# Optimization experiments

Hardware: AMD Instinct MI355X
Metric: run time of the kernel (lower is better)

Reference implementation:

```python
import jax, jax.numpy as jnp
import numpy as np

EPS = 1e-8  # matches torch F.cosine_similarity eps


def setup_inputs() -> dict:
    key = jax.random.key(0)
    k1, = jax.random.split(key, 1)
    N, U, D = 512, 32, 512
    embeddings = jax.random.normal(k1, (N, U, D), dtype=jnp.float32)
    w = jnp.asarray(10.0, dtype=jnp.float32)  # init_w
    b = jnp.asarray(-5.0, dtype=jnp.float32)  # init_b
    return {"embeddings": embeddings, "w": w, "b": b}


def reference(embeddings, w, b):
    N, U, D = embeddings.shape
    # centroids per speaker (mean over utterances; module includes current utt)
    centroids = embeddings.mean(axis=1)  # (N, D)
    # cosine similarity via normalize + matmul
    e = embeddings.reshape(N * U, D)
    e_n = e / jnp.maximum(jnp.linalg.norm(e, axis=-1, keepdims=True), EPS)
    c_n = centroids / jnp.maximum(
        jnp.linalg.norm(centroids, axis=-1, keepdims=True), EPS)
    sim = (e_n @ c_n.T).reshape(N, U, N)  # (N, U, N)
    sim = w * sim + b
    logp = jax.nn.log_softmax(sim, axis=-1)  # (N, U, N)
    # pick logp[j, k, j] for every j, k
    diag = jnp.take_along_axis(
        logp, jnp.arange(N)[:, None, None], axis=2)[..., 0]  # (N, U)
    return -diag.mean()
```

## Files before the change

kernel.cpp:

```cpp
#include <hip/hip_runtime.h>
#include <math.h>

#define N_SPK 512
#define N_UTT 32
#define DIM   512
#define EPSN  1e-8f

typedef __attribute__((ext_vector_type(8))) short  short8;
typedef __attribute__((ext_vector_type(4))) float  f32x4;

__device__ inline unsigned short f2bf(float x) {
  unsigned int u = __builtin_bit_cast(unsigned int, x);
  unsigned int r = (u + 0x7fffu + ((u >> 16) & 1u)) >> 16;
  return (unsigned short)r;
}

#define CNK_ELEMS (N_SPK * DIM)

__global__ __launch_bounds__(256) void centroid_kernel(
    const float* __restrict__ emb, unsigned short* __restrict__ cnk) {
  int j = blockIdx.x, t = threadIdx.x;
  int c4 = t & 127, half = t >> 7;
  const float4* base = (const float4*)(emb + (size_t)j * N_UTT * DIM);
  float4 s = {0.f, 0.f, 0.f, 0.f};
#pragma unroll
  for (int u = 0; u < 16; ++u) {
    float4 v = base[(half + 2 * u) * 128 + c4];
    s.x += v.x; s.y += v.y; s.z += v.z; s.w += v.w;
  }
  __shared__ float4 comb[128];
  if (half) comb[c4] = s;
  __syncthreads();
  float4 m = {0.f, 0.f, 0.f, 0.f};
  float ss = 0.f;
  if (!half) {
    float4 o = comb[c4];
    m.x = (s.x + o.x) * (1.f / N_UTT);
    m.y = (s.y + o.y) * (1.f / N_UTT);
    m.z = (s.z + o.z) * (1.f / N_UTT);
    m.w = (s.w + o.w) * (1.f / N_UTT);
    ss = m.x * m.x + m.y * m.y + m.z * m.z + m.w * m.w;
  }
#pragma unroll
  for (int off = 32; off > 0; off >>= 1) ss += __shfl_xor(ss, off, 64);
  __shared__ float red[4];
  if ((t & 63) == 0) red[t >> 6] = ss;
  __syncthreads();
  float total = red[0] + red[1] + red[2] + red[3];
  float inv = 1.f / fmaxf(sqrtf(total), EPSN);
  if (!half) {
    int d0 = c4 * 4;
    int kc = d0 >> 5;
    unsigned short* p = cnk + ((size_t)kc * N_SPK + j) * 32 + (d0 & 31);
    p[0] = f2bf(m.x * inv); p[1] = f2bf(m.y * inv);
    p[2] = f2bf(m.z * inv); p[3] = f2bf(m.w * inv);
  }
}

__global__ __launch_bounds__(512, 4) void ge2e_kernel(
    const float* __restrict__ emb, const unsigned short* __restrict__ cnk,
    const float* __restrict__ wp, const float* __restrict__ bp,
    float* __restrict__ partials) {
  __shared__ __align__(16) unsigned short E[N_UTT * DIM];
  __shared__ float red[8][N_UTT][2];
  __shared__ float dred[8];

  int j = blockIdx.x;
  int t = threadIdx.x;
  int lane = t & 63, wid = t >> 6;
  int n15 = lane & 15, quad = lane >> 4;

#pragma unroll
  for (int r8 = 0; r8 < 4; ++r8) {
    int r = wid * 4 + r8;
    const float* rp = emb + ((size_t)j * N_UTT + r) * DIM + lane * 8;
    float4 v0 = *(const float4*)rp;
    float4 v1 = *(const float4*)(rp + 4);
    float ss = v0.x * v0.x + v0.y * v0.y + v0.z * v0.z + v0.w * v0.w +
               v1.x * v1.x + v1.y * v1.y + v1.z * v1.z + v1.w * v1.w;
#pragma unroll
    for (int off = 32; off > 0; off >>= 1) ss += __shfl_xor(ss, off, 64);
    float inv = 1.f / fmaxf(sqrtf(ss), EPSN);
    short8 pk;
    pk[0] = (short)f2bf(v0.x * inv); pk[1] = (short)f2bf(v0.y * inv);
    pk[2] = (short)f2bf(v0.z * inv); pk[3] = (short)f2bf(v0.w * inv);
    pk[4] = (short)f2bf(v1.x * inv); pk[5] = (short)f2bf(v1.y * inv);
    pk[6] = (short)f2bf(v1.z * inv); pk[7] = (short)f2bf(v1.w * inv);
    int sw = lane ^ (r & 7);
    *(short8*)&E[r * DIM + sw * 8] = pk;
  }
  __syncthreads();

  f32x4 acc[2][4];
#pragma unroll
  for (int mt = 0; mt < 2; ++mt)
#pragma unroll
    for (int nt = 0; nt < 4; ++nt) acc[mt][nt] = (f32x4){0.f, 0.f, 0.f, 0.f};

  for (int ks = 0; ks < 16; ++ks) {
    short8 b[4];
#pragma unroll
    for (int nt = 0; nt < 4; ++nt) {
      int c = wid * 64 + nt * 16 + n15;
      b[nt] = *(const short8*)(cnk + ((size_t)ks * N_SPK + c) * 32 + quad * 8);
    }
    short8 a[2];
#pragma unroll
    for (int mt = 0; mt < 2; ++mt) {
      int r = mt * 16 + n15;
      int sw = (ks * 4 + quad) ^ (r & 7);
      a[mt] = *(const short8*)&E[r * DIM + sw * 8];
    }
#pragma unroll
    for (int mt = 0; mt < 2; ++mt)
#pragma unroll
      for (int nt = 0; nt < 4; ++nt)
        acc[mt][nt] = __builtin_amdgcn_mfma_f32_16x16x32_bf16(
            a[mt], b[nt], acc[mt][nt], 0, 0, 0);
  }

  float w = *wp, bb = *bp;
  float dsum = 0.f;
#pragma unroll
  for (int mt = 0; mt < 2; ++mt)
#pragma unroll
    for (int nt = 0; nt < 4; ++nt) {
      int c = wid * 64 + nt * 16 + n15;
      bool isdiag = (c == j);
#pragma unroll
      for (int rg = 0; rg < 4; ++rg) {
        float v = fmaf(w, acc[mt][nt][rg], bb);
        acc[mt][nt][rg] = v;
        if (isdiag) dsum += v;
      }
    }

#pragma unroll
  for (int mt = 0; mt < 2; ++mt)
#pragma unroll
    for (int rg = 0; rg < 4; ++rg) {
      float m = -INFINITY;
#pragma unroll
      for (int nt = 0; nt < 4; ++nt) m = fmaxf(m, acc[mt][nt][rg]);
#pragma unroll
      for (int off = 1; off < 16; off <<= 1) m = fmaxf(m, __shfl_xor(m, off, 64));
      float s = 0.f;
#pragma unroll
      for (int nt = 0; nt < 4; ++nt) s += __expf(acc[mt][nt][rg] - m);
#pragma unroll
      for (int off = 1; off < 16; off <<= 1) s += __shfl_xor(s, off, 64);
      if (n15 == 0) {
        int r = mt * 16 + quad * 4 + rg;
        red[wid][r][0] = m;
        red[wid][r][1] = s;
      }
    }
#pragma unroll
  for (int off = 32; off > 0; off >>= 1) dsum += __shfl_xor(dsum, off, 64);
  if (lane == 0) dred[wid] = dsum;
  __syncthreads();

  if (t < 32) {
    float M = -INFINITY;
#pragma unroll
    for (int ww = 0; ww < 8; ++ww) M = fmaxf(M, red[ww][t][0]);
    float S = 0.f;
#pragma unroll
    for (int ww = 0; ww < 8; ++ww) S += red[ww][t][1] * __expf(red[ww][t][0] - M);
    float lse = M + __logf(S);
#pragma unroll
    for (int off = 16; off > 0; off >>= 1) lse += __shfl_xor(lse, off, 64);
    if (t == 0) {
      float d = dred[0] + dred[1] + dred[2] + dred[3] +
                dred[4] + dred[5] + dred[6] + dred[7];
      partials[j] = lse - d;
    }
  }
}

__global__ __launch_bounds__(512) void finalize_kernel(
    const float* __restrict__ partials, float* __restrict__ out) {
  int t = threadIdx.x;
  float v = partials[t];
#pragma unroll
  for (int off = 32; off > 0; off >>= 1) v += __shfl_xor(v, off, 64);
  __shared__ float r[8];
  if ((t & 63) == 0) r[t >> 6] = v;
  __syncthreads();
  if (t == 0) {
    float s = r[0] + r[1] + r[2] + r[3] + r[4] + r[5] + r[6] + r[7];
    out[0] = s * (1.f / (N_SPK * N_UTT));
  }
}

extern "C" void kernel_launch(void* const* d_in, const int* in_sizes, int n_in,
                              void* d_out, int out_size, void* d_ws, size_t ws_size,
                              hipStream_t stream) {
  const float* emb = (const float*)d_in[0];
  const float* wp  = (const float*)d_in[1];
  const float* bp  = (const float*)d_in[2];
  float* out = (float*)d_out;
  unsigned short* cnk = (unsigned short*)d_ws;
  float* partials = (float*)((char*)d_ws + (size_t)CNK_ELEMS * 2);

  centroid_kernel<<<N_SPK, 256, 0, stream>>>(emb, cnk);
  ge2e_kernel<<<N_SPK, 512, 0, stream>>>(emb, cnk, wp, bp, partials);
  finalize_kernel<<<1, 512, 0, stream>>>(partials, out);
}
```

Baseline: 97.33 us.

## Double ge2e block threads and fold finalize into last-block atomic reduction

The main kernel now runs 1024 threads (16 waves) per speaker block, so each wave handles 32 centroid columns and 2 normalization rows instead of 64 and 4. The separate finalize launch is removed: every block atomically increments a counter, which the centroid kernel resets, and the last block to arrive sums the partials and writes the output. This is meant to raise parallelism per block and save one kernel launch. In exchange it adds atomic and fence overhead, and the 1024-thread launch bound with 8 blocks requested may limit registers per thread.

```diff
diff --git a/kernel.cpp b/kernel.cpp
--- a/kernel.cpp
+++ b/kernel.cpp
@@ -18,8 +18,10 @@
 #define CNK_ELEMS (N_SPK * DIM)
 
 __global__ __launch_bounds__(256) void centroid_kernel(
-    const float* __restrict__ emb, unsigned short* __restrict__ cnk) {
+    const float* __restrict__ emb, unsigned short* __restrict__ cnk,
+    unsigned int* __restrict__ counter) {
   int j = blockIdx.x, t = threadIdx.x;
+  if (j == 0 && t == 0) *counter = 0;
   int c4 = t & 127, half = t >> 7;
   const float4* base = (const float4*)(emb + (size_t)j * N_UTT * DIM);
   float4 s = {0.f, 0.f, 0.f, 0.f};
@@ -57,13 +59,16 @@
   }
 }
 
-__global__ __launch_bounds__(512, 4) void ge2e_kernel(
+__global__ __launch_bounds__(1024, 8) void ge2e_kernel(
     const float* __restrict__ emb, const unsigned short* __restrict__ cnk,
     const float* __restrict__ wp, const float* __restrict__ bp,
-    float* __restrict__ partials) {
+    float* __restrict__ partials, unsigned int* __restrict__ counter,
+    float* __restrict__ out) {
   __shared__ __align__(16) unsigned short E[N_UTT * DIM];
-  __shared__ float red[8][N_UTT][2];
-  __shared__ float dred[8];
+  __shared__ float red[16][N_UTT][2];
+  __shared__ float dred[16];
+  __shared__ float nred[16];
+  __shared__ int amLast;
 
   int j = blockIdx.x;
   int t = threadIdx.x;
@@ -71,8 +76,8 @@
   int n15 = lane & 15, quad = lane >> 4;
 
 #pragma unroll
-  for (int r8 = 0; r8 < 4; ++r8) {
-    int r = wid * 4 + r8;
+  for (int r8 = 0; r8 < 2; ++r8) {
+    int r = wid * 2 + r8;
     const float* rp = emb + ((size_t)j * N_UTT + r) * DIM + lane * 8;
     float4 v0 = *(const float4*)rp;
     float4 v1 = *(const float4*)(rp + 4);
@@ -91,17 +96,18 @@
   }
   __syncthreads();
 
-  f32x4 acc[2][4];
+  f32x4 acc[2][2];
 #pragma unroll
   for (int mt = 0; mt < 2; ++mt)
 #pragma unroll
-    for (int nt = 0; nt < 4; ++nt) acc[mt][nt] = (f32x4){0.f, 0.f, 0.f, 0.f};
-
+    for (int nt = 0; nt < 2; ++nt) acc[mt][nt] = (f32x4){0.f, 0.f, 0.f, 0.f};
+
+#pragma unroll 4
   for (int ks = 0; ks < 16; ++ks) {
-    short8 b[4];
-#pragma unroll
-    for (int nt = 0; nt < 4; ++nt) {
-      int c = wid * 64 + nt * 16 + n15;
+    short8 b[2];
+#pragma unroll
+    for (int nt = 0; nt < 2; ++nt) {
+      int c = wid * 32 + nt * 16 + n15;
       b[nt] = *(const short8*)(cnk + ((size_t)ks * N_SPK + c) * 32 + quad * 8);
     }
     short8 a[2];
@@ -114,7 +120,7 @@
 #pragma unroll
     for (int mt = 0; mt < 2; ++mt)
 #pragma unroll
-      for (int nt = 0; nt < 4; ++nt)
+      for (int nt = 0; nt < 2; ++nt)
         acc[mt][nt] = __builtin_amdgcn_mfma_f32_16x16x32_bf16(
             a[mt], b[nt], acc[mt][nt], 0, 0, 0);
   }
@@ -124,8 +130,8 @@
 #pragma unroll
   for (int mt = 0; mt < 2; ++mt)
 #pragma unroll
-    for (int nt = 0; nt < 4; ++nt) {
-      int c = wid * 64 + nt * 16 + n15;
+    for (int nt = 0; nt < 2; ++nt) {
+      int c = wid * 32 + nt * 16 + n15;
       bool isdiag = (c == j);
 #pragma unroll
       for (int rg = 0; rg < 4; ++rg) {
@@ -141,12 +147,12 @@
     for (int rg = 0; rg < 4; ++rg) {
       float m = -INFINITY;
 #pragma unroll
-      for (int nt = 0; nt < 4; ++nt) m = fmaxf(m, acc[mt][nt][rg]);
+      for (int nt = 0; nt < 2; ++nt) m = fmaxf(m, acc[mt][nt][rg]);
 #pragma unroll
       for (int off = 1; off < 16; off <<= 1) m = fmaxf(m, __shfl_xor(m, off, 64));
       float s = 0.f;
 #pragma unroll
-      for (int nt = 0; nt < 4; ++nt) s += __expf(acc[mt][nt][rg] - m);
+      for (int nt = 0; nt < 2; ++nt) s += __expf(acc[mt][nt][rg] - m);
 #pragma unroll
       for (int off = 1; off < 16; off <<= 1) s += __shfl_xor(s, off, 64);
       if (n15 == 0) {
@@ -163,33 +169,41 @@
   if (t < 32) {
     float M = -INFINITY;
 #pragma unroll
-    for (int ww = 0; ww < 8; ++ww) M = fmaxf(M, red[ww][t][0]);
+    for (int ww = 0; ww < 16; ++ww) M = fmaxf(M, red[ww][t][0]);
     float S = 0.f;
 #pragma unroll
-    for (int ww = 0; ww < 8; ++ww) S += red[ww][t][1] * __expf(red[ww][t][0] - M);
+    for (int ww = 0; ww < 16; ++ww)
+      S += red[ww][t][1] * __expf(red[ww][t][0] - M);
     float lse = M + __logf(S);
 #pragma unroll
     for (int off = 16; off > 0; off >>= 1) lse += __shfl_xor(lse, off, 64);
     if (t == 0) {
-      float d = dred[0] + dred[1] + dred[2] + dred[3] +
-                dred[4] + dred[5] + dred[6] + dred[7];
+      float d = 0.f;
+#pragma unroll
+      for (int ww = 0; ww < 16; ++ww) d += dred[ww];
       partials[j] = lse - d;
     }
   }
-}
-
-__global__ __launch_bounds__(512) void finalize_kernel(
-    const float* __restrict__ partials, float* __restrict__ out) {
-  int t = threadIdx.x;
-  float v = partials[t];
-#pragma unroll
-  for (int off = 32; off > 0; off >>= 1) v += __shfl_xor(v, off, 64);
-  __shared__ float r[8];
-  if ((t & 63) == 0) r[t >> 6] = v;
-  __syncthreads();
+
   if (t == 0) {
-    float s = r[0] + r[1] + r[2] + r[3] + r[4] + r[5] + r[6] + r[7];
-    out[0] = s * (1.f / (N_SPK * N_UTT));
+    __threadfence();
+    unsigned int old = atomicAdd(counter, 1u);
+    amLast = (old == (unsigned int)(gridDim.x - 1));
+  }
+  __syncthreads();
+  if (amLast) {
+    __threadfence();
+    float v = (t < N_SPK) ? partials[t] : 0.f;
+#pragma unroll
+    for (int off = 32; off > 0; off >>= 1) v += __shfl_xor(v, off, 64);
+    if (lane == 0) nred[wid] = v;
+    __syncthreads();
+    if (t == 0) {
+      float s = 0.f;
+#pragma unroll
+      for (int ww = 0; ww < 16; ++ww) s += nred[ww];
+      out[0] = s * (1.f / (N_SPK * N_UTT));
+    }
   }
 }
 
@@ -202,8 +216,10 @@
   float* out = (float*)d_out;
   unsigned short* cnk = (unsigned short*)d_ws;
   float* partials = (float*)((char*)d_ws + (size_t)CNK_ELEMS * 2);
-
-  centroid_kernel<<<N_SPK, 256, 0, stream>>>(emb, cnk);
-  ge2e_kernel<<<N_SPK, 512, 0, stream>>>(emb, cnk, wp, bp, partials);
-  finalize_kernel<<<1, 512, 0, stream>>>(partials, out);
-}
+  unsigned int* counter =
+      (unsigned int*)((char*)d_ws + (size_t)CNK_ELEMS * 2 + N_SPK * 4);
+
+  centroid_kernel<<<N_SPK, 256, 0, stream>>>(emb, cnk, counter);
+  ge2e_kernel<<<N_SPK, 1024, 0, stream>>>(emb, cnk, wp, bp, partials, counter,
+                                          out);
+}
```

Result: slower. 108.0 us (+10.9%).

## Fold normalization into prep kernel, stage bf16 embeddings, fuse finalize via atomic counter

Applied to the files above, without the earlier changes.

A single prep kernel now computes each speaker's centroid and also writes the row-normalized bf16 embeddings (already swizzled) to a workspace buffer. The ge2e kernel then only copies those bf16 rows into LDS instead of reading fp32 and normalizing. The separate finalize launch is replaced by a last-block-done pattern using an atomic counter. This reads the fp32 embeddings once instead of twice and removes one kernel launch, but adds a 16 MB bf16 write and read-back plus threadfence/atomic overhead.

```diff
diff --git a/kernel.cpp b/kernel.cpp
--- a/kernel.cpp
+++ b/kernel.cpp
@@ -15,60 +15,21 @@
   return (unsigned short)r;
 }
 
-#define CNK_ELEMS (N_SPK * DIM)
-
-__global__ __launch_bounds__(256) void centroid_kernel(
-    const float* __restrict__ emb, unsigned short* __restrict__ cnk) {
+#define CNK_BYTES ((size_t)N_SPK * DIM * 2)
+#define EG_BYTES  ((size_t)N_SPK * N_UTT * DIM * 2)
+
+__global__ __launch_bounds__(512) void prep_kernel(
+    const float* __restrict__ emb, unsigned short* __restrict__ cnk,
+    unsigned short* __restrict__ Eg, unsigned int* __restrict__ counter) {
+  __shared__ float colsum[8][DIM];
+  __shared__ float nred[8];
   int j = blockIdx.x, t = threadIdx.x;
-  int c4 = t & 127, half = t >> 7;
-  const float4* base = (const float4*)(emb + (size_t)j * N_UTT * DIM);
-  float4 s = {0.f, 0.f, 0.f, 0.f};
-#pragma unroll
-  for (int u = 0; u < 16; ++u) {
-    float4 v = base[(half + 2 * u) * 128 + c4];
-    s.x += v.x; s.y += v.y; s.z += v.z; s.w += v.w;
-  }
-  __shared__ float4 comb[128];
-  if (half) comb[c4] = s;
-  __syncthreads();
-  float4 m = {0.f, 0.f, 0.f, 0.f};
-  float ss = 0.f;
-  if (!half) {
-    float4 o = comb[c4];
-    m.x = (s.x + o.x) * (1.f / N_UTT);
-    m.y = (s.y + o.y) * (1.f / N_UTT);
-    m.z = (s.z + o.z) * (1.f / N_UTT);
-    m.w = (s.w + o.w) * (1.f / N_UTT);
-    ss = m.x * m.x + m.y * m.y + m.z * m.z + m.w * m.w;
-  }
-#pragma unroll
-  for (int off = 32; off > 0; off >>= 1) ss += __shfl_xor(ss, off, 64);
-  __shared__ float red[4];
-  if ((t & 63) == 0) red[t >> 6] = ss;
-  __syncthreads();
-  float total = red[0] + red[1] + red[2] + red[3];
-  float inv = 1.f / fmaxf(sqrtf(total), EPSN);
-  if (!half) {
-    int d0 = c4 * 4;
-    int kc = d0 >> 5;
-    unsigned short* p = cnk + ((size_t)kc * N_SPK + j) * 32 + (d0 & 31);
-    p[0] = f2bf(m.x * inv); p[1] = f2bf(m.y * inv);
-    p[2] = f2bf(m.z * inv); p[3] = f2bf(m.w * inv);
-  }
-}
-
-__global__ __launch_bounds__(512, 4) void ge2e_kernel(
-    const float* __restrict__ emb, const unsigned short* __restrict__ cnk,
-    const float* __restrict__ wp, const float* __restrict__ bp,
-    float* __restrict__ partials) {
-  __shared__ __align__(16) unsigned short E[N_UTT * DIM];
-  __shared__ float red[8][N_UTT][2];
-  __shared__ float dred[8];
-
-  int j = blockIdx.x;
-  int t = threadIdx.x;
   int lane = t & 63, wid = t >> 6;
-  int n15 = lane & 15, quad = lane >> 4;
+  if (j == 0 && t == 0) *counter = 0;
+
+  float cs[8];
+#pragma unroll
+  for (int i = 0; i < 8; ++i) cs[i] = 0.f;
 
 #pragma unroll
   for (int r8 = 0; r8 < 4; ++r8) {
@@ -76,6 +37,8 @@
     const float* rp = emb + ((size_t)j * N_UTT + r) * DIM + lane * 8;
     float4 v0 = *(const float4*)rp;
     float4 v1 = *(const float4*)(rp + 4);
+    cs[0] += v0.x; cs[1] += v0.y; cs[2] += v0.z; cs[3] += v0.w;
+    cs[4] += v1.x; cs[5] += v1.y; cs[6] += v1.z; cs[7] += v1.w;
     float ss = v0.x * v0.x + v0.y * v0.y + v0.z * v0.z + v0.w * v0.w +
                v1.x * v1.x + v1.y * v1.y + v1.z * v1.z + v1.w * v1.w;
 #pragma unroll
@@ -87,8 +50,48 @@
     pk[4] = (short)f2bf(v1.x * inv); pk[5] = (short)f2bf(v1.y * inv);
     pk[6] = (short)f2bf(v1.z * inv); pk[7] = (short)f2bf(v1.w * inv);
     int sw = lane ^ (r & 7);
-    *(short8*)&E[r * DIM + sw * 8] = pk;
-  }
+    *(short8*)&Eg[((size_t)j * N_UTT + r) * DIM + sw * 8] = pk;
+  }
+  *(float4*)&colsum[wid][lane * 8] = (float4){cs[0], cs[1], cs[2], cs[3]};
+  *(float4*)&colsum[wid][lane * 8 + 4] = (float4){cs[4], cs[5], cs[6], cs[7]};
+  __syncthreads();
+
+  float c = 0.f;
+#pragma unroll
+  for (int ww = 0; ww < 8; ++ww) c += colsum[ww][t];
+  c *= (1.f / N_UTT);
+  float ss = c * c;
+#pragma unroll
+  for (int off = 32; off > 0; off >>= 1) ss += __shfl_xor(ss, off, 64);
+  if (lane == 0) nred[wid] = ss;
+  __syncthreads();
+  float total = nred[0] + nred[1] + nred[2] + nred[3] +
+                nred[4] + nred[5] + nred[6] + nred[7];
+  float cinv = 1.f / fmaxf(sqrtf(total), EPSN);
+  cnk[((size_t)(t >> 5) * N_SPK + j) * 32 + (t & 31)] = f2bf(c * cinv);
+}
+
+__global__ __launch_bounds__(512, 4) void ge2e_kernel(
+    const unsigned short* __restrict__ Eg,
+    const unsigned short* __restrict__ cnk,
+    const float* __restrict__ wp, const float* __restrict__ bp,
+    float* __restrict__ partials, unsigned int* __restrict__ counter,
+    float* __restrict__ out) {
+  __shared__ __align__(16) unsigned short E[N_UTT * DIM];
+  __shared__ float red[8][N_UTT][2];
+  __shared__ float dred[8];
+  __shared__ float nred[8];
+  __shared__ int amLast;
+
+  int j = blockIdx.x;
+  int t = threadIdx.x;
+  int lane = t & 63, wid = t >> 6;
+  int n15 = lane & 15, quad = lane >> 4;
+
+  const int4* src = (const int4*)(Eg + (size_t)j * N_UTT * DIM);
+  int4* dst = (int4*)E;
+#pragma unroll
+  for (int i = 0; i < 4; ++i) dst[i * 512 + t] = src[i * 512 + t];
   __syncthreads();
 
   f32x4 acc[2][4];
@@ -176,20 +179,25 @@
       partials[j] = lse - d;
     }
   }
-}
-
-__global__ __launch_bounds__(512) void finalize_kernel(
-    const float* __restrict__ partials, float* __restrict__ out) {
-  int t = threadIdx.x;
-  float v = partials[t];
-#pragma unroll
-  for (int off = 32; off > 0; off >>= 1) v += __shfl_xor(v, off, 64);
-  __shared__ float r[8];
-  if ((t & 63) == 0) r[t >> 6] = v;
-  __syncthreads();
+
   if (t == 0) {
-    float s = r[0] + r[1] + r[2] + r[3] + r[4] + r[5] + r[6] + r[7];
-    out[0] = s * (1.f / (N_SPK * N_UTT));
+    __threadfence();
+    unsigned int old = atomicAdd(counter, 1u);
+    amLast = (old == (unsigned int)(gridDim.x - 1));
+  }
+  __syncthreads();
+  if (amLast) {
+    __threadfence();
+    float v = partials[t];
+#pragma unroll
+    for (int off = 32; off > 0; off >>= 1) v += __shfl_xor(v, off, 64);
+    if (lane == 0) nred[wid] = v;
+    __syncthreads();
+    if (t == 0) {
+      float s = nred[0] + nred[1] + nred[2] + nred[3] +
+                nred[4] + nred[5] + nred[6] + nred[7];
+      out[0] = s * (1.f / (N_SPK * N_UTT));
+    }
   }
 }
 
@@ -201,9 +209,12 @@
   const float* bp  = (const float*)d_in[2];
   float* out = (float*)d_out;
   unsigned short* cnk = (unsigned short*)d_ws;
-  float* partials = (float*)((char*)d_ws + (size_t)CNK_ELEMS * 2);
-
-  centroid_kernel<<<N_SPK, 256, 0, stream>>>(emb, cnk);
-  ge2e_kernel<<<N_SPK, 512, 0, stream>>>(emb, cnk, wp, bp, partials);
-  finalize_kernel<<<1, 512, 0, stream>>>(partials, out);
-}
+  unsigned short* Eg  = (unsigned short*)((char*)d_ws + CNK_BYTES);
+  float* partials = (float*)((char*)d_ws + CNK_BYTES + EG_BYTES);
+  unsigned int* counter =
+      (unsigned int*)((char*)d_ws + CNK_BYTES + EG_BYTES + N_SPK * 4);
+
+  prep_kernel<<<N_SPK, 512, 0, stream>>>(emb, cnk, Eg, counter);
+  ge2e_kernel<<<N_SPK, 512, 0, stream>>>(Eg, cnk, wp, bp, partials, counter,
+                                         out);
+}
```

Result: slower. 112.0 us (+15.0%).

## Split similarity kernel across column halves and widen centroid blocks

Applied to the files above, without the earlier changes.

The main kernel now launches two blocks per speaker, each covering half of the centroid columns. Each block writes per-row partial max and sum-exp pairs, and the finalize kernel merges them into the log-sum-exp. The centroid kernel uses 1024 threads with an 8-way row split to spread its loads across more threads. The aim is more blocks to occupy the GPU, at the cost of reloading and normalizing each speaker's embeddings twice and a heavier finalize step.

```diff
diff --git a/kernel.cpp b/kernel.cpp
--- a/kernel.cpp
+++ b/kernel.cpp
@@ -15,42 +15,44 @@
   return (unsigned short)r;
 }
 
-#define CNK_ELEMS (N_SPK * DIM)
-
-__global__ __launch_bounds__(256) void centroid_kernel(
-    const float* __restrict__ emb, unsigned short* __restrict__ cnk) {
+#define CNK_BYTES ((size_t)N_SPK * DIM * 2)
+#define MS_BYTES  ((size_t)1024 * N_UTT * 2 * 4)
+
+__global__ void centroid_kernel(const float* __restrict__ emb,
+                                unsigned short* __restrict__ cnk) {
+  __shared__ float4 colsum[8][128];
+  __shared__ float nred[2];
   int j = blockIdx.x, t = threadIdx.x;
-  int c4 = t & 127, half = t >> 7;
+  int c4 = t & 127, rg = t >> 7;
   const float4* base = (const float4*)(emb + (size_t)j * N_UTT * DIM);
   float4 s = {0.f, 0.f, 0.f, 0.f};
 #pragma unroll
-  for (int u = 0; u < 16; ++u) {
-    float4 v = base[(half + 2 * u) * 128 + c4];
+  for (int u = 0; u < 4; ++u) {
+    float4 v = base[(rg + 8 * u) * 128 + c4];
     s.x += v.x; s.y += v.y; s.z += v.z; s.w += v.w;
   }
-  __shared__ float4 comb[128];
-  if (half) comb[c4] = s;
-  __syncthreads();
-  float4 m = {0.f, 0.f, 0.f, 0.f};
-  float ss = 0.f;
-  if (!half) {
-    float4 o = comb[c4];
-    m.x = (s.x + o.x) * (1.f / N_UTT);
-    m.y = (s.y + o.y) * (1.f / N_UTT);
-    m.z = (s.z + o.z) * (1.f / N_UTT);
-    m.w = (s.w + o.w) * (1.f / N_UTT);
-    ss = m.x * m.x + m.y * m.y + m.z * m.z + m.w * m.w;
-  }
-#pragma unroll
-  for (int off = 32; off > 0; off >>= 1) ss += __shfl_xor(ss, off, 64);
-  __shared__ float red[4];
-  if ((t & 63) == 0) red[t >> 6] = ss;
-  __syncthreads();
-  float total = red[0] + red[1] + red[2] + red[3];
-  float inv = 1.f / fmaxf(sqrtf(total), EPSN);
-  if (!half) {
-    int d0 = c4 * 4;
-    int kc = d0 >> 5;
+  colsum[rg][c4] = s;
+  __syncthreads();
+  if (t < 128) {
+    float4 m = {0.f, 0.f, 0.f, 0.f};
+#pragma unroll
+    for (int g = 0; g < 8; ++g) {
+      float4 v = colsum[g][t];
+      m.x += v.x; m.y += v.y; m.z += v.z; m.w += v.w;
+    }
+    m.x *= (1.f / N_UTT); m.y *= (1.f / N_UTT);
+    m.z *= (1.f / N_UTT); m.w *= (1.f / N_UTT);
+    float ss = m.x * m.x + m.y * m.y + m.z * m.z + m.w * m.w;
+#pragma unroll
+    for (int off = 32; off > 0; off >>= 1) ss += __shfl_xor(ss, off, 64);
+    if ((t & 63) == 0) nred[t >> 6] = ss;
+    colsum[0][t] = m;
+  }
+  __syncthreads();
+  if (t < 128) {
+    float4 m = colsum[0][t];
+    float inv = 1.f / fmaxf(sqrtf(nred[0] + nred[1]), EPSN);
+    int d0 = t * 4, kc = d0 >> 5;
     unsigned short* p = cnk + ((size_t)kc * N_SPK + j) * 32 + (d0 & 31);
     p[0] = f2bf(m.x * inv); p[1] = f2bf(m.y * inv);
     p[2] = f2bf(m.z * inv); p[3] = f2bf(m.w * inv);
@@ -60,12 +62,13 @@
 __global__ __launch_bounds__(512, 4) void ge2e_kernel(
     const float* __restrict__ emb, const unsigned short* __restrict__ cnk,
     const float* __restrict__ wp, const float* __restrict__ bp,
-    float* __restrict__ partials) {
+    float2* __restrict__ ms, float* __restrict__ dsum_g) {
   __shared__ __align__(16) unsigned short E[N_UTT * DIM];
   __shared__ float red[8][N_UTT][2];
   __shared__ float dred[8];
 
-  int j = blockIdx.x;
+  int bid = blockIdx.x;
+  int j = bid >> 1, h = bid & 1;
   int t = threadIdx.x;
   int lane = t & 63, wid = t >> 6;
   int n15 = lane & 15, quad = lane >> 4;
@@ -91,17 +94,18 @@
   }
   __syncthreads();
 
-  f32x4 acc[2][4];
+  int cbase = h * 256 + wid * 32;
+  f32x4 acc[2][2];
 #pragma unroll
   for (int mt = 0; mt < 2; ++mt)
 #pragma unroll
-    for (int nt = 0; nt < 4; ++nt) acc[mt][nt] = (f32x4){0.f, 0.f, 0.f, 0.f};
+    for (int nt = 0; nt < 2; ++nt) acc[mt][nt] = (f32x4){0.f, 0.f, 0.f, 0.f};
 
   for (int ks = 0; ks < 16; ++ks) {
-    short8 b[4];
-#pragma unroll
-    for (int nt = 0; nt < 4; ++nt) {
-      int c = wid * 64 + nt * 16 + n15;
+    short8 b[2];
+#pragma unroll
+    for (int nt = 0; nt < 2; ++nt) {
+      int c = cbase + nt * 16 + n15;
       b[nt] = *(const short8*)(cnk + ((size_t)ks * N_SPK + c) * 32 + quad * 8);
     }
     short8 a[2];
@@ -114,7 +118,7 @@
 #pragma unroll
     for (int mt = 0; mt < 2; ++mt)
 #pragma unroll
-      for (int nt = 0; nt < 4; ++nt)
+      for (int nt = 0; nt < 2; ++nt)
         acc[mt][nt] = __builtin_amdgcn_mfma_f32_16x16x32_bf16(
             a[mt], b[nt], acc[mt][nt], 0, 0, 0);
   }
@@ -124,8 +128,8 @@
 #pragma unroll
   for (int mt = 0; mt < 2; ++mt)
 #pragma unroll
-    for (int nt = 0; nt < 4; ++nt) {
-      int c = wid * 64 + nt * 16 + n15;
+    for (int nt = 0; nt < 2; ++nt) {
+      int c = cbase + nt * 16 + n15;
       bool isdiag = (c == j);
 #pragma unroll
       for (int rg = 0; rg < 4; ++rg) {
@@ -141,12 +145,12 @@
     for (int rg = 0; rg < 4; ++rg) {
       float m = -INFINITY;
 #pragma unroll
-      for (int nt = 0; nt < 4; ++nt) m = fmaxf(m, acc[mt][nt][rg]);
+      for (int nt = 0; nt < 2; ++nt) m = fmaxf(m, acc[mt][nt][rg]);
 #pragma unroll
       for (int off = 1; off < 16; off <<= 1) m = fmaxf(m, __shfl_xor(m, off, 64));
       float s = 0.f;
 #pragma unroll
-      for (int nt = 0; nt < 4; ++nt) s += __expf(acc[mt][nt][rg] - m);
+      for (int nt = 0; nt < 2; ++nt) s += __expf(acc[mt][nt][rg] - m);
 #pragma unroll
       for (int off = 1; off < 16; off <<= 1) s += __shfl_xor(s, off, 64);
       if (n15 == 0) {
@@ -167,28 +171,38 @@
     float S = 0.f;
 #pragma unroll
     for (int ww = 0; ww < 8; ++ww) S += red[ww][t][1] * __expf(red[ww][t][0] - M);
-    float lse = M + __logf(S);
-#pragma unroll
-    for (int off = 16; off > 0; off >>= 1) lse += __shfl_xor(lse, off, 64);
+    ms[(size_t)bid * N_UTT + t] = make_float2(M, S);
     if (t == 0) {
       float d = dred[0] + dred[1] + dred[2] + dred[3] +
                 dred[4] + dred[5] + dred[6] + dred[7];
-      partials[j] = lse - d;
+      dsum_g[bid] = d;
     }
   }
 }
 
 __global__ __launch_bounds__(512) void finalize_kernel(
-    const float* __restrict__ partials, float* __restrict__ out) {
+    const float2* __restrict__ ms, const float* __restrict__ dsum_g,
+    float* __restrict__ out) {
   int t = threadIdx.x;
-  float v = partials[t];
+  const float2* m0 = ms + (size_t)(2 * t) * N_UTT;
+  const float2* m1 = m0 + N_UTT;
+  float acc = 0.f;
+#pragma unroll 8
+  for (int r = 0; r < N_UTT; ++r) {
+    float2 a = m0[r], b = m1[r];
+    float M = fmaxf(a.x, b.x);
+    float S = a.y * __expf(a.x - M) + b.y * __expf(b.x - M);
+    acc += M + __logf(S);
+  }
+  acc -= dsum_g[2 * t] + dsum_g[2 * t + 1];
+  float v = acc;
 #pragma unroll
   for (int off = 32; off > 0; off >>= 1) v += __shfl_xor(v, off, 64);
-  __shared__ float r[8];
-  if ((t & 63) == 0) r[t >> 6] = v;
+  __shared__ float r8[8];
+  if ((t & 63) == 0) r8[t >> 6] = v;
   __syncthreads();
   if (t == 0) {
-    float s = r[0] + r[1] + r[2] + r[3] + r[4] + r[5] + r[6] + r[7];
+    float s = r8[0] + r8[1] + r8[2] + r8[3] + r8[4] + r8[5] + r8[6] + r8[7];
     out[0] = s * (1.f / (N_SPK * N_UTT));
   }
 }
@@ -201,9 +215,10 @@
   const float* bp  = (const float*)d_in[2];
   float* out = (float*)d_out;
   unsigned short* cnk = (unsigned short*)d_ws;
-  float* partials = (float*)((char*)d_ws + (size_t)CNK_ELEMS * 2);
-
-  centroid_kernel<<<N_SPK, 256, 0, stream>>>(emb, cnk);
-  ge2e_kernel<<<N_SPK, 512, 0, stream>>>(emb, cnk, wp, bp, partials);
-  finalize_kernel<<<1, 512, 0, stream>>>(partials, out);
-}
+  float2* ms   = (float2*)((char*)d_ws + CNK_BYTES);
+  float* dsum_g = (float*)((char*)d_ws + CNK_BYTES + MS_BYTES);
+
+  centroid_kernel<<<N_SPK, 1024, 0, stream>>>(emb, cnk);
+  ge2e_kernel<<<2 * N_SPK, 512, 0, stream>>>(emb, cnk, wp, bp, ms, dsum_g);
+  finalize_kernel<<<1, 512, 0, stream>>>(ms, dsum_g, out);
+}
```

New measurement: 113.5 us. 16.7% more time.
